# Performance work log

Hardware: AMD Instinct MI355X
Metric: run time of the kernel (lower is better)

Reference implementation:

```python
import jax, jax.numpy as jnp
import numpy as np

N, CH, H, W = 4, 512, 64, 64
FEAT, NUM_K, POOL_PER = 256, 64, 128
POOL = NUM_K * POOL_PER  # 8192 total concept slots


def setup_inputs() -> dict:
    key = jax.random.key(0)
    k_x, k_t, k_o, k_p = jax.random.split(key, 4)
    x = jax.random.normal(k_x, (N, CH, H, W), dtype=jnp.float32)
    # 1x1 conv weights stored as [out, in] matrices (kernel_size=1, bias=False)
    w_theta = jax.random.normal(k_t, (FEAT, CH), dtype=jnp.float32) * 0.02
    w_o = jax.random.normal(k_o, (CH, FEAT), dtype=jnp.float32) * 0.02
    # concept pool buffer initialized with torch.rand -> uniform [0, 1)
    concept_pool = jax.random.uniform(k_p, (FEAT, POOL), dtype=jnp.float32)
    gamma = jnp.float32(0.5)  # learned scalar gate (init 0.0 in module; 0.5 to exercise the path)
    return {"x": x, "w_theta": w_theta, "w_o": w_o, "concept_pool": concept_pool, "gamma": gamma}


def reference(x, w_theta, w_o, concept_pool, gamma):
    # Concept attention: queries from theta 1x1 conv, keys/values are the
    # external concept pool memory [feature_dim, total_pool_size].
    n, c, h, w = x.shape
    hw = h * w
    # theta 1x1 conv: [n, ch, h, w] -> [n, feat, hw]
    theta = jnp.einsum('nchw,fc->nfhw', x, w_theta).reshape(n, FEAT, hw)
    # attention logits over pool slots: [n, hw, pool]
    logits = jnp.einsum('nfl,fp->nlp', theta, concept_pool)
    attn = jax.nn.softmax(logits, axis=-1)
    # aggregate pool values: [n, feat, hw]
    agg = jnp.einsum('nlp,fp->nfl', attn, concept_pool).reshape(n, FEAT, h, w)
    # output 1x1 conv back to ch, gated residual
    o = jnp.einsum('nfhw,cf->nchw', agg, w_o)
    return x + gamma * o
```

## Files before the change

### kernel.cpp

```cpp
#include <hip/hip_runtime.h>

#define NB 4
#define CHN 512
#define HWD 4096
#define LTOT (NB*HWD)
#define FEAT_ 256
#define POOL_ 8192

typedef __attribute__((ext_vector_type(8))) __bf16 bf16x8;
typedef __attribute__((ext_vector_type(8))) unsigned short u16x8;
typedef __attribute__((ext_vector_type(8))) _Float16 f16x8;
typedef __attribute__((ext_vector_type(4))) unsigned u32x4;
typedef __attribute__((ext_vector_type(4))) float f32x4;
typedef __attribute__((ext_vector_type(16))) float f32x16;

static __device__ __forceinline__ float fexp2(float x){
  return __builtin_amdgcn_exp2f(x);
}

static __device__ __forceinline__ unsigned short f2bf(float f){
  union { float f; unsigned u; } c; c.f = f;
  unsigned u = c.u;
  u += 0x7fffu + ((u >> 16) & 1u);
  return (unsigned short)(u >> 16);
}

static __device__ __forceinline__ unsigned pk_f16(float lo, float hi){
  auto r = __builtin_amdgcn_cvt_pkrtz(lo, hi);
  return __builtin_bit_cast(unsigned, r);
}

static __device__ __forceinline__ f32x4 mfma16(bf16x8 a, bf16x8 b, f32x4 c){
  return __builtin_amdgcn_mfma_f32_16x16x32_bf16(a, b, c, 0, 0, 0);
}
static __device__ __forceinline__ f32x16 mfma32b(bf16x8 a, bf16x8 b, f32x16 c){
  return __builtin_amdgcn_mfma_f32_32x32x16_bf16(a, b, c, 0, 0, 0);
}
static __device__ __forceinline__ f32x16 mfma32h(f16x8 a, f16x8 b, f32x16 c){
  return __builtin_amdgcn_mfma_f32_32x32x16_f16(a, b, c, 0, 0, 0);
}

static __device__ __forceinline__ bf16x8 ld_bf8(const void* p){
  u16x8 v = *(const u16x8*)p;
  return __builtin_bit_cast(bf16x8, v);
}
static __device__ __forceinline__ f16x8 ld_f8(const void* p){
  u16x8 v = *(const u16x8*)p;
  return __builtin_bit_cast(f16x8, v);
}

static __device__ __forceinline__ void gload16(const void* g, void* l){
  __builtin_amdgcn_global_load_lds((const __attribute__((address_space(1))) void*)g,
                                   (__attribute__((address_space(3))) void*)l, 16, 0, 0);
}

__global__ void k_cvt(const float* __restrict__ src, unsigned short* __restrict__ dst, int n4){
  int i = blockIdx.x * 256 + threadIdx.x;
  if (i < n4) {
    const float4 v = *(const float4*)(src + (size_t)i * 4);
    ushort4 o; o.x = f2bf(v.x); o.y = f2bf(v.y); o.z = f2bf(v.z); o.w = f2bf(v.w);
    *(ushort4*)(dst + (size_t)i * 4) = o;
  }
}

__global__ __launch_bounds__(256) void k_poolKF(const float* __restrict__ pool,
                                                unsigned short* __restrict__ poolKF){
  int t = blockIdx.x >> 2;
  int tid = threadIdx.x;
  int kc = ((blockIdx.x & 3) << 2) | (tid >> 6);
  int lane = tid & 63;
  int p = t*32 + (lane & 31);
  int f0 = kc*16 + (lane >> 5)*8;
  u16x8 o;
  #pragma unroll
  for (int j = 0; j < 8; ++j) o[j] = f2bf(pool[(size_t)(f0+j)*POOL_ + p]);
  *(u16x8*)((char*)poolKF + (size_t)t*16384 + kc*1024 + lane*16) = o;
}

__global__ __launch_bounds__(256) void k_poolVF(const float* __restrict__ pool,
                                                _Float16* __restrict__ poolVF){
  int t = blockIdx.x >> 2;
  int tid = threadIdx.x;
  int g = ((blockIdx.x & 3) << 2) | (tid >> 6);
  int lane = tid & 63;
  int f = (g & 7)*32 + (lane & 31);
  int ph = g >> 3, h2 = lane >> 5;
  f16x8 o;
  #pragma unroll
  for (int j = 0; j < 8; ++j) {
    int po = (j & 3) + 8*(j >> 2) + 4*h2 + 16*ph;
    o[j] = (_Float16)pool[(size_t)f*POOL_ + t*32 + po];
  }
  *(f16x8*)((char*)poolVF + (size_t)t*16384 + g*1024 + lane*16) = o;
}

__global__ __launch_bounds__(256) void k_xT(const float* __restrict__ x,
                                            unsigned short* __restrict__ xT){
  __shared__ float tile[32][33];
  int b = blockIdx.x;
  int lt = b & 127; int ct = (b >> 7) & 15; int n = b >> 11;
  int t = threadIdx.x;
  int fi = t >> 3, j = (t & 7) * 4;
  const float4 v = *(const float4*)(x + ((size_t)(n*CHN + ct*32 + fi)) * HWD + lt*32 + j);
  tile[fi][j+0] = v.x; tile[fi][j+1] = v.y; tile[fi][j+2] = v.z; tile[fi][j+3] = v.w;
  __syncthreads();
  int pi = t >> 3, fj = (t & 7) * 4;
  ushort4 o;
  o.x = f2bf(tile[fj+0][pi]); o.y = f2bf(tile[fj+1][pi]);
  o.z = f2bf(tile[fj+2][pi]); o.w = f2bf(tile[fj+3][pi]);
  *(ushort4*)((char*)xT + ((size_t)(n*HWD + lt*32 + pi)) * 1024 + (ct*32 + fj) * 2) = o;
}

__global__ __launch_bounds__(256) void k_theta(const unsigned short* __restrict__ xT,
                                               const unsigned short* __restrict__ wt,
                                               unsigned short* __restrict__ Q){
  int w = threadIdx.x >> 6, lane = threadIdx.x & 63;
  int lq = lane & 15, hq = lane >> 4;
  int lbase = blockIdx.x * 64 + w * 16;
  const char* xb = (const char*)xT;
  const char* wb = (const char*)wt;
  f32x4 acc[16];
  #pragma unroll
  for (int i = 0; i < 16; ++i) acc[i] = {};
  #pragma unroll 2
  for (int kk = 0; kk < 16; ++kk) {
    bf16x8 a = ld_bf8(xb + (size_t)(lbase + lq) * 1024 + kk*64 + hq*16);
    #pragma unroll
    for (int fi = 0; fi < 16; ++fi) {
      bf16x8 bfr = ld_bf8(wb + (size_t)(fi*16 + lq) * 1024 + kk*64 + hq*16);
      acc[fi] = mfma16(a, bfr, acc[fi]);
    }
  }
  #pragma unroll
  for (int fi = 0; fi < 16; ++fi) {
    #pragma unroll
    for (int r = 0; r < 4; ++r) {
      int l = lbase + hq*4 + r;
      Q[(size_t)l * 256 + fi*16 + lq] = f2bf(acc[fi][r] * 1.44269504f);
    }
  }
}

__global__ __launch_bounds__(256, 2) void k_attn(const unsigned short* __restrict__ Qg,
                                                 const unsigned short* __restrict__ poolKF,
                                                 const _Float16* __restrict__ poolVF,
                                                 _Float16* __restrict__ accP,
                                                 float* __restrict__ pm,
                                                 float* __restrict__ ps){
  __shared__ __attribute__((aligned(16))) unsigned short K_lds[2][32*256];
  __shared__ __attribute__((aligned(16))) _Float16 V_lds[2][8192];
  __shared__ float Sc[4][32];
  __shared__ float As[4][32];

  int w = threadIdx.x >> 6, lane = threadIdx.x & 63;
  int ln = lane & 31, h2 = lane >> 5;
  int qblock = blockIdx.x & 127, slice = blockIdx.x >> 7;
  int qa0 = qblock * 128 + w * 32;

  const char* qp = (const char*)Qg;
  bf16x8 qf[16];
  #pragma unroll
  for (int kc = 0; kc < 16; ++kc)
    qf[kc] = ld_bf8(qp + (size_t)(qa0 + ln) * 512 + kc*32 + h2*16);

  f32x16 acc32[8];
  #pragma unroll
  for (int i = 0; i < 8; ++i) acc32[i] = {};
  float accs = 0.0f;
  float m = -__builtin_inff();

  const char* ktb = (const char*)poolKF;
  const char* vnb = (const char*)poolVF;
  int kds[4];
  #pragma unroll
  for (int i = 0; i < 4; ++i) kds[i] = (w*4 + i) * 1024;
  int lsrc = lane * 16;

  {
    size_t tb = (size_t)(slice * 64) * 16384;
    #pragma unroll
    for (int i = 0; i < 4; ++i) {
      gload16(ktb + tb + kds[i] + lsrc, (char*)K_lds[0] + kds[i]);
      gload16(vnb + tb + kds[i] + lsrc, (char*)V_lds[0] + kds[i]);
    }
  }
  __syncthreads();

  int cur = 0;
  for (int t = 0; t < 64; ++t) {
    if (t < 63) {
      size_t tb = (size_t)(slice*64 + t + 1) * 16384;
      #pragma unroll
      for (int i = 0; i < 4; ++i) {
        gload16(ktb + tb + kds[i] + lsrc, (char*)K_lds[cur^1] + kds[i]);
        gload16(vnb + tb + kds[i] + lsrc, (char*)V_lds[cur^1] + kds[i]);
      }
    }

    const char* Kb = (const char*)K_lds[cur] + lsrc;
    const char* Vb = (const char*)V_lds[cur] + lsrc;

    f32x16 Sa = {}, Sb = {};
    #pragma unroll
    for (int kc = 0; kc < 8; ++kc) {
      bf16x8 k0 = ld_bf8(Kb + (2*kc)*1024);
      bf16x8 k1 = ld_bf8(Kb + (2*kc+1)*1024);
      Sa = mfma32b(k0, qf[2*kc], Sa);
      Sb = mfma32b(k1, qf[2*kc+1], Sb);
    }
    float S[16];
    #pragma unroll
    for (int r = 0; r < 16; ++r) S[r] = Sa[r] + Sb[r];

    float px = S[0];
    #pragma unroll
    for (int r = 1; r < 16; ++r) px = fmaxf(px, S[r]);
    px = fmaxf(px, __shfl_xor(px, 32));

    if (__any((int)(px > m + 5.5f))) {
      float mn = fmaxf(m, px);
      float sc = fexp2(m - mn);
      m = mn;
      accs *= sc;
      if (lane < 32) Sc[w][lane] = sc;
      f32x4 s4[4];
      #pragma unroll
      for (int blk = 0; blk < 4; ++blk)
        s4[blk] = *(const f32x4*)&Sc[w][8*blk + 4*h2];
      #pragma unroll
      for (int fb = 0; fb < 8; ++fb)
        #pragma unroll
        for (int r = 0; r < 16; ++r)
          acc32[fb][r] *= s4[r>>2][r&3];
    }

    float Pr[16];
    #pragma unroll
    for (int r = 0; r < 16; ++r) Pr[r] = fexp2(S[r] - m);
    float sum = (((Pr[0]+Pr[1])+(Pr[2]+Pr[3])) + ((Pr[4]+Pr[5])+(Pr[6]+Pr[7])))
              + (((Pr[8]+Pr[9])+(Pr[10]+Pr[11])) + ((Pr[12]+Pr[13])+(Pr[14]+Pr[15])));
    sum += __shfl_xor(sum, 32);
    accs += sum;
    u32x4 w0, w1;
    #pragma unroll
    for (int j = 0; j < 4; ++j) {
      w0[j] = pk_f16(Pr[2*j],   Pr[2*j+1]);
      w1[j] = pk_f16(Pr[8+2*j], Pr[8+2*j+1]);
    }
    f16x8 pa0 = __builtin_bit_cast(f16x8, w0);
    f16x8 pa1 = __builtin_bit_cast(f16x8, w1);

    #pragma unroll
    for (int fb = 0; fb < 8; ++fb) {
      f16x8 v0 = ld_f8(Vb + fb*1024);
      acc32[fb] = mfma32h(pa0, v0, acc32[fb]);
    }
    #pragma unroll
    for (int fb = 0; fb < 8; ++fb) {
      f16x8 v1 = ld_f8(Vb + (8 + fb)*1024);
      acc32[fb] = mfma32h(pa1, v1, acc32[fb]);
    }

    __syncthreads();
    cur ^= 1;
  }

  if (lane < 32) As[w][lane] = accs;
  float inv[16];
  #pragma unroll
  for (int blk = 0; blk < 4; ++blk) {
    f32x4 a4 = *(const f32x4*)&As[w][8*blk + 4*h2];
    inv[blk*4+0] = 1.0f / a4[0]; inv[blk*4+1] = 1.0f / a4[1];
    inv[blk*4+2] = 1.0f / a4[2]; inv[blk*4+3] = 1.0f / a4[3];
  }
  size_t sbase = (size_t)slice * 16384 + qa0;
  #pragma unroll
  for (int fb = 0; fb < 8; ++fb) {
    #pragma unroll
    for (int r = 0; r < 16; ++r) {
      int q = (r & 3) + 8*(r >> 2) + 4*h2;
      accP[(sbase + q) * 256 + fb*32 + ln] = (_Float16)(acc32[fb][r] * inv[r]);
    }
  }
  if (lane < 32) {
    pm[sbase + lane] = m;
    ps[sbase + lane] = accs;
  }
}

__global__ __launch_bounds__(256) void k_comb(const _Float16* __restrict__ accP,
                                              const float* __restrict__ pm,
                                              const float* __restrict__ ps,
                                              unsigned short* __restrict__ agg){
  int q = blockIdx.x * 16 + (threadIdx.x >> 4);
  int f0 = (threadIdx.x & 15) * 16;
  float m0 = pm[q], m1 = pm[16384 + q], m2 = pm[2*16384 + q], m3 = pm[3*16384 + q];
  float M = fmaxf(fmaxf(m0, m1), fmaxf(m2, m3));
  float w0 = fexp2(m0 - M) * ps[q];
  float w1 = fexp2(m1 - M) * ps[16384 + q];
  float w2 = fexp2(m2 - M) * ps[2*16384 + q];
  float w3 = fexp2(m3 - M) * ps[3*16384 + q];
  float inv = 1.0f / (w0 + w1 + w2 + w3);
  w0 *= inv; w1 *= inv; w2 *= inv; w3 *= inv;
  const _Float16* a0 = accP + (size_t)q * 256 + f0;
  #pragma unroll
  for (int j = 0; j < 16; j += 8) {
    f16x8 v0 = *(const f16x8*)(a0 + j);
    f16x8 v1 = *(const f16x8*)(a0 + j + (size_t)16384*256);
    f16x8 v2 = *(const f16x8*)(a0 + j + (size_t)2*16384*256);
    f16x8 v3 = *(const f16x8*)(a0 + j + (size_t)3*16384*256);
    u16x8 o;
    #pragma unroll
    for (int k = 0; k < 8; ++k) {
      float s = w0*(float)v0[k] + w1*(float)v1[k] + w2*(float)v2[k] + w3*(float)v3[k];
      o[k] = f2bf(s);
    }
    *(u16x8*)(agg + (size_t)q * 256 + f0 + j) = o;
  }
}

__global__ __launch_bounds__(256) void k_out(const float* __restrict__ x,
                                             const unsigned short* __restrict__ wo,
                                             const unsigned short* __restrict__ agg,
                                             const float* __restrict__ gammap,
                                             float* __restrict__ out){
  int w = threadIdx.x >> 6, lane = threadIdx.x & 63;
  int lq = lane & 15, hq = lane >> 4;
  int b = blockIdx.x;
  int lg = b & 63, cg = (b >> 6) & 7, n = b >> 9;
  const char* wb = (const char*)wo;
  const char* ab = (const char*)agg;
  f32x4 acc[4];
  #pragma unroll
  for (int i = 0; i < 4; ++i) acc[i] = {};
  int crow = cg*64 + w*16 + lq;
  #pragma unroll
  for (int kk = 0; kk < 8; ++kk) {
    bf16x8 a = ld_bf8(wb + (size_t)crow * 512 + kk*64 + hq*16);
    #pragma unroll
    for (int li = 0; li < 4; ++li) {
      bf16x8 bb = ld_bf8(ab + (size_t)(n*HWD + lg*64 + li*16 + lq) * 512 + kk*64 + hq*16);
      acc[li] = mfma16(a, bb, acc[li]);
    }
  }
  float g = gammap[0];
  #pragma unroll
  for (int li = 0; li < 4; ++li) {
    #pragma unroll
    for (int r = 0; r < 4; ++r) {
      int c = cg*64 + w*16 + hq*4 + r;
      int l = lg*64 + li*16 + lq;
      size_t idx = ((size_t)(n*CHN + c)) * HWD + l;
      out[idx] = x[idx] + g * acc[li][r];
    }
  }
}

extern "C" void kernel_launch(void* const* d_in, const int* in_sizes, int n_in,
                              void* d_out, int out_size, void* d_ws, size_t ws_size,
                              hipStream_t stream) {
  const float* x     = (const float*)d_in[0];
  const float* wt    = (const float*)d_in[1];
  const float* wo    = (const float*)d_in[2];
  const float* pool  = (const float*)d_in[3];
  const float* gamma = (const float*)d_in[4];
  char* ws = (char*)d_ws;
  unsigned short* wt_b  = (unsigned short*)(ws + 0);
  unsigned short* wo_b  = (unsigned short*)(ws + 262144);
  _Float16*       poolVF= (_Float16*)(ws + 524288);
  unsigned short* poolKF= (unsigned short*)(ws + 4718592);
  unsigned short* Qb    = (unsigned short*)(ws + 8912896);
  unsigned short* aggb  = (unsigned short*)(ws + 17301504);
  unsigned short* xT    = (unsigned short*)(ws + 25690112);
  _Float16*       accP  = (_Float16*)(ws + 25690112);
  float*          pm    = (float*)(ws + 59244544);
  float*          ps    = (float*)(ws + 59506688);
  float* out = (float*)d_out;

  k_cvt<<<dim3(128), dim3(256), 0, stream>>>(wt, wt_b, 32768);
  k_cvt<<<dim3(128), dim3(256), 0, stream>>>(wo, wo_b, 32768);
  k_poolVF<<<dim3(1024), dim3(256), 0, stream>>>(pool, poolVF);
  k_poolKF<<<dim3(1024), dim3(256), 0, stream>>>(pool, poolKF);
  k_xT<<<dim3(8192), dim3(256), 0, stream>>>(x, xT);
  k_theta<<<dim3(256), dim3(256), 0, stream>>>(xT, wt_b, Qb);
  k_attn<<<dim3(512), dim3(256), 0, stream>>>(Qb, poolKF, poolVF, accP, pm, ps);
  k_comb<<<dim3(1024), dim3(256), 0, stream>>>(accP, pm, ps, aggb);
  k_out<<<dim3(2048), dim3(256), 0, stream>>>(x, wo_b, aggb, gamma, out);
}
```

Before: 246.5 us.

## Software-pipeline PV MFMA one tile behind QK using triple-buffered V in LDS

Restructures the attention loop so the P·V MFMAs for tile t-1 are issued at the start of iteration t, overlapping them with the QK MFMAs and softmax of tile t. To make this safe, V tiles move to a three-slot LDS ring while K stays double-buffered, and a final P·V step is added after the loop. The per-row rescale factors and final normalizers are now broadcast with cross-lane shuffles instead of a round trip through LDS, and the row max uses a tree reduction. The extra V slot raises LDS use per block, which may limit how many blocks fit on a CU.

```diff
diff --git a/kernel.cpp b/kernel.cpp
--- a/kernel.cpp
+++ b/kernel.cpp
@@ -148,9 +148,7 @@
                                                  float* __restrict__ pm,
                                                  float* __restrict__ ps){
   __shared__ __attribute__((aligned(16))) unsigned short K_lds[2][32*256];
-  __shared__ __attribute__((aligned(16))) _Float16 V_lds[2][8192];
-  __shared__ float Sc[4][32];
-  __shared__ float As[4][32];
+  __shared__ __attribute__((aligned(16))) _Float16 V_lds[3][8192];
 
   int w = threadIdx.x >> 6, lane = threadIdx.x & 63;
   int ln = lane & 31, h2 = lane >> 5;
@@ -168,6 +166,7 @@
   for (int i = 0; i < 8; ++i) acc32[i] = {};
   float accs = 0.0f;
   float m = -__builtin_inff();
+  f16x8 pa0 = {}, pa1 = {};
 
   const char* ktb = (const char*)poolKF;
   const char* vnb = (const char*)poolVF;
@@ -186,20 +185,29 @@
   }
   __syncthreads();
 
-  int cur = 0;
   for (int t = 0; t < 64; ++t) {
+    if (t > 0) {
+      const char* Vb = (const char*)V_lds[(t-1)%3] + lsrc;
+      #pragma unroll
+      for (int fb = 0; fb < 8; ++fb)
+        acc32[fb] = mfma32h(pa0, ld_f8(Vb + fb*1024), acc32[fb]);
+      #pragma unroll
+      for (int fb = 0; fb < 8; ++fb)
+        acc32[fb] = mfma32h(pa1, ld_f8(Vb + (8 + fb)*1024), acc32[fb]);
+    }
+
     if (t < 63) {
       size_t tb = (size_t)(slice*64 + t + 1) * 16384;
+      char* Kd = (char*)K_lds[(t+1) & 1];
+      char* Vd = (char*)V_lds[(t+1) % 3];
       #pragma unroll
       for (int i = 0; i < 4; ++i) {
-        gload16(ktb + tb + kds[i] + lsrc, (char*)K_lds[cur^1] + kds[i]);
-        gload16(vnb + tb + kds[i] + lsrc, (char*)V_lds[cur^1] + kds[i]);
+        gload16(ktb + tb + kds[i] + lsrc, Kd + kds[i]);
+        gload16(vnb + tb + kds[i] + lsrc, Vd + kds[i]);
       }
     }
 
-    const char* Kb = (const char*)K_lds[cur] + lsrc;
-    const char* Vb = (const char*)V_lds[cur] + lsrc;
-
+    const char* Kb = (const char*)K_lds[t & 1] + lsrc;
     f32x16 Sa = {}, Sb = {};
     #pragma unroll
     for (int kc = 0; kc < 8; ++kc) {
@@ -212,9 +220,12 @@
     #pragma unroll
     for (int r = 0; r < 16; ++r) S[r] = Sa[r] + Sb[r];
 
-    float px = S[0];
-    #pragma unroll
-    for (int r = 1; r < 16; ++r) px = fmaxf(px, S[r]);
+    float x0 = fmaxf(S[0], S[1]),  x1 = fmaxf(S[2], S[3]);
+    float x2 = fmaxf(S[4], S[5]),  x3 = fmaxf(S[6], S[7]);
+    float x4 = fmaxf(S[8], S[9]),  x5 = fmaxf(S[10], S[11]);
+    float x6 = fmaxf(S[12], S[13]), x7 = fmaxf(S[14], S[15]);
+    float px = fmaxf(fmaxf(fmaxf(x0, x1), fmaxf(x2, x3)),
+                     fmaxf(fmaxf(x4, x5), fmaxf(x6, x7)));
     px = fmaxf(px, __shfl_xor(px, 32));
 
     if (__any((int)(px > m + 5.5f))) {
@@ -222,16 +233,13 @@
       float sc = fexp2(m - mn);
       m = mn;
       accs *= sc;
-      if (lane < 32) Sc[w][lane] = sc;
-      f32x4 s4[4];
       #pragma unroll
-      for (int blk = 0; blk < 4; ++blk)
-        s4[blk] = *(const f32x4*)&Sc[w][8*blk + 4*h2];
-      #pragma unroll
-      for (int fb = 0; fb < 8; ++fb)
+      for (int r = 0; r < 16; ++r) {
+        int qsrc = (r & 3) + 8*(r >> 2) + 4*h2 + (lane & 32);
+        float s = __shfl(sc, qsrc);
         #pragma unroll
-        for (int r = 0; r < 16; ++r)
-          acc32[fb][r] *= s4[r>>2][r&3];
+        for (int fb = 0; fb < 8; ++fb) acc32[fb][r] *= s;
+      }
     }
 
     float Pr[16];
@@ -247,31 +255,27 @@
       w0[j] = pk_f16(Pr[2*j],   Pr[2*j+1]);
       w1[j] = pk_f16(Pr[8+2*j], Pr[8+2*j+1]);
     }
-    f16x8 pa0 = __builtin_bit_cast(f16x8, w0);
-    f16x8 pa1 = __builtin_bit_cast(f16x8, w1);
-
-    #pragma unroll
-    for (int fb = 0; fb < 8; ++fb) {
-      f16x8 v0 = ld_f8(Vb + fb*1024);
-      acc32[fb] = mfma32h(pa0, v0, acc32[fb]);
-    }
-    #pragma unroll
-    for (int fb = 0; fb < 8; ++fb) {
-      f16x8 v1 = ld_f8(Vb + (8 + fb)*1024);
-      acc32[fb] = mfma32h(pa1, v1, acc32[fb]);
-    }
+    pa0 = __builtin_bit_cast(f16x8, w0);
+    pa1 = __builtin_bit_cast(f16x8, w1);
 
     __syncthreads();
-    cur ^= 1;
-  }
-
-  if (lane < 32) As[w][lane] = accs;
+  }
+
+  {
+    const char* Vb = (const char*)V_lds[63 % 3] + lsrc;
+    #pragma unroll
+    for (int fb = 0; fb < 8; ++fb)
+      acc32[fb] = mfma32h(pa0, ld_f8(Vb + fb*1024), acc32[fb]);
+    #pragma unroll
+    for (int fb = 0; fb < 8; ++fb)
+      acc32[fb] = mfma32h(pa1, ld_f8(Vb + (8 + fb)*1024), acc32[fb]);
+  }
+
   float inv[16];
   #pragma unroll
-  for (int blk = 0; blk < 4; ++blk) {
-    f32x4 a4 = *(const f32x4*)&As[w][8*blk + 4*h2];
-    inv[blk*4+0] = 1.0f / a4[0]; inv[blk*4+1] = 1.0f / a4[1];
-    inv[blk*4+2] = 1.0f / a4[2]; inv[blk*4+3] = 1.0f / a4[3];
+  for (int r = 0; r < 16; ++r) {
+    int qsrc = (r & 3) + 8*(r >> 2) + 4*h2 + (lane & 32);
+    inv[r] = 1.0f / __shfl(accs, qsrc);
   }
   size_t sbase = (size_t)slice * 16384 + qa0;
   #pragma unroll
```

Result: slower. 254.2 us (+3.1%).
